# Performance work log

Measured on AMD Instinct MI355X. Metric: run time of the kernel, lower is better.

Reference implementation:

```python
import jax, jax.numpy as jnp
import numpy as np

DIM = 512
NUM_HEADS = 16
HEAD_DIM = DIM // NUM_HEADS
HIDDEN = int(DIM * 4.0)
EPS = 1e-5


def layer_norm(x, gamma, beta):
    mu = jnp.mean(x, axis=-1, keepdims=True)
    var = jnp.mean(jnp.square(x - mu), axis=-1, keepdims=True)
    return (x - mu) * jax.lax.rsqrt(var + EPS) * gamma + beta


def setup_inputs() -> dict:
    key = jax.random.key(0)
    ks = jax.random.split(key, 8)
    B, L, C = 32, 3136, DIM
    x = jax.random.normal(ks[0], (B, L, C), dtype=jnp.float32)
    norm1_g = jnp.ones((C,), jnp.float32)
    norm1_b = jnp.zeros((C,), jnp.float32)
    # spatial (per-head) mixing weight: (num_heads, head_dim, head_dim)
    w_spatial = jax.random.normal(ks[1], (NUM_HEADS, HEAD_DIM, HEAD_DIM), jnp.float32) * (1.0 / np.sqrt(HEAD_DIM))
    norm2_g = jnp.ones((C,), jnp.float32)
    norm2_b = jnp.zeros((C,), jnp.float32)
    w1 = jax.random.normal(ks[2], (C, HIDDEN), jnp.float32) * (1.0 / np.sqrt(C))
    b1 = jnp.zeros((HIDDEN,), jnp.float32)
    w2 = jax.random.normal(ks[3], (HIDDEN, C), jnp.float32) * (1.0 / np.sqrt(HIDDEN))
    b2 = jnp.zeros((C,), jnp.float32)
    return {"x": x, "norm1_g": norm1_g, "norm1_b": norm1_b, "w_spatial": w_spatial,
            "norm2_g": norm2_g, "norm2_b": norm2_b, "w1": w1, "b1": b1, "w2": w2, "b2": b2}


def reference(x, norm1_g, norm1_b, w_spatial, norm2_g, norm2_b, w1, b1, w2, b2):
    B, L, C = x.shape
    shortcut = x
    h = layer_norm(x, norm1_g, norm1_b)
    # window partition -> per-head channel-sub-dim linear (shared across windows/positions)
    # mathematically equivalent to applying the per-head matmul at every token
    h = h.reshape(B, L, NUM_HEADS, HEAD_DIM)
    h = jnp.einsum('blhd,hde->blhe', h, w_spatial)
    h = h.reshape(B, L, C)
    x = shortcut + h
    # channel MLP: Linear -> GELU(tanh) -> Linear
    y = layer_norm(x, norm2_g, norm2_b)
    y = jax.nn.gelu(y @ w1 + b1, approximate=True)
    y = y @ w2 + b2
    return x + y
```

## Files before the change

kernel.cpp:

```cpp
#include <hip/hip_runtime.h>
#include <hip/hip_bf16.h>


typedef __bf16 bf16x8 __attribute__((ext_vector_type(8)));
typedef float f32x4 __attribute__((ext_vector_type(4)));

constexpr int CDIM = 512;
constexpr int HID = 2048;
constexpr int MROWS = 32 * 3136;
constexpr float LN_EPS = 1e-5f;

static __device__ __forceinline__ float gelu_tanh(float x) {
  const float u = 0.7978845608028654f * fmaf(0.044715f * x * x, x, x);
  const float e = __expf(2.0f * u);
  return 0.5f * x * (2.0f - 2.0f / (e + 1.0f));
}

static __device__ __forceinline__ void load_lds16(const void* g, void* l) {
  __builtin_amdgcn_global_load_lds((__attribute__((address_space(1))) void*)g,
                                   (__attribute__((address_space(3))) void*)l,
                                   16, 0, 0);
}

template <int KD, int ND>
__global__ __launch_bounds__(256) void cvt_t(const float* __restrict__ src,
                                             __hip_bfloat16* __restrict__ dst) {
  __shared__ float tl[64][65];
  const int t = threadIdx.x;
  constexpr int NTN = ND / 64;
  const int k0 = (blockIdx.x / NTN) * 64;
  const int n0 = (blockIdx.x % NTN) * 64;
  const int c4 = (t & 15) * 4;
  const int r = t >> 4;
#pragma unroll
  for (int j = 0; j < 4; ++j) {
    const int kk = r + j * 16;
    const float4 v = *(const float4*)&src[(size_t)(k0 + kk) * ND + n0 + c4];
    tl[c4 + 0][kk] = v.x;
    tl[c4 + 1][kk] = v.y;
    tl[c4 + 2][kk] = v.z;
    tl[c4 + 3][kk] = v.w;
  }
  __syncthreads();
#pragma unroll
  for (int j = 0; j < 4; ++j) {
    const int nn = r + j * 16;
    __hip_bfloat16 o[4];
#pragma unroll
    for (int c = 0; c < 4; ++c) o[c] = __float2bfloat16(tl[nn][c4 + c]);
    *(uint2*)&dst[(size_t)(n0 + nn) * KD + k0 + c4] = *(const uint2*)o;
  }
}

__global__ __launch_bounds__(256) void fused_pre(
    const float* __restrict__ x, const float* __restrict__ g1,
    const float* __restrict__ b1, const float* __restrict__ wsp,
    const float* __restrict__ g2, const float* __restrict__ b2,
    float* __restrict__ x2out, __hip_bfloat16* __restrict__ yout) {
  __shared__ float lnbuf[2][CDIM];
  __shared__ float red[16];

  const int t = threadIdx.x;
  const int lane = t & 63;
  const int w = t >> 6;
  const int c0 = 2 * t;
  const int hd = c0 >> 5, e0 = c0 & 31;

  float wc0[32], wc1[32];
#pragma unroll
  for (int d = 0; d < 32; ++d) {
    const float2 wv = *(const float2*)&wsp[(hd * 32 + d) * 32 + e0];
    wc0[d] = wv.x;
    wc1[d] = wv.y;
  }
  const float2 g1v = *(const float2*)&g1[c0];
  const float2 b1v = *(const float2*)&b1[c0];
  const float2 g2v = *(const float2*)&g2[c0];
  const float2 b2v = *(const float2*)&b2[c0];

  for (int rp = blockIdx.x; rp < MROWS / 2; rp += gridDim.x) {
    const size_t ra = (size_t)rp * 2, rb = ra + 1;
    const float2 xa = *(const float2*)&x[ra * CDIM + c0];
    const float2 xb = *(const float2*)&x[rb * CDIM + c0];

    float sa = xa.x + xa.y, qa = xa.x * xa.x + xa.y * xa.y;
    float sb = xb.x + xb.y, qb = xb.x * xb.x + xb.y * xb.y;
#pragma unroll
    for (int off = 32; off; off >>= 1) {
      sa += __shfl_down(sa, off);
      qa += __shfl_down(qa, off);
      sb += __shfl_down(sb, off);
      qb += __shfl_down(qb, off);
    }
    if (lane == 0) {
      red[w * 4 + 0] = sa;
      red[w * 4 + 1] = qa;
      red[w * 4 + 2] = sb;
      red[w * 4 + 3] = qb;
    }
    __syncthreads();
    sa = red[0] + red[4] + red[8] + red[12];
    qa = red[1] + red[5] + red[9] + red[13];
    sb = red[2] + red[6] + red[10] + red[14];
    qb = red[3] + red[7] + red[11] + red[15];
    float mua = sa * (1.0f / CDIM), mub = sb * (1.0f / CDIM);
    float rsa = rsqrtf(qa * (1.0f / CDIM) - mua * mua + LN_EPS);
    float rsb = rsqrtf(qb * (1.0f / CDIM) - mub * mub + LN_EPS);
    lnbuf[0][c0] = (xa.x - mua) * rsa * g1v.x + b1v.x;
    lnbuf[0][c0 + 1] = (xa.y - mua) * rsa * g1v.y + b1v.y;
    lnbuf[1][c0] = (xb.x - mub) * rsb * g1v.x + b1v.x;
    lnbuf[1][c0 + 1] = (xb.y - mub) * rsb * g1v.y + b1v.y;
    __syncthreads();

    float ha0 = 0.f, ha1 = 0.f, hb0 = 0.f, hb1 = 0.f;
#pragma unroll
    for (int d = 0; d < 32; ++d) {
      const float la = lnbuf[0][hd * 32 + d];
      const float lb = lnbuf[1][hd * 32 + d];
      ha0 = fmaf(la, wc0[d], ha0);
      ha1 = fmaf(la, wc1[d], ha1);
      hb0 = fmaf(lb, wc0[d], hb0);
      hb1 = fmaf(lb, wc1[d], hb1);
    }
    const float a0 = xa.x + ha0, a1 = xa.y + ha1;
    const float b0 = xb.x + hb0, b1r = xb.y + hb1;
    float2 av;
    av.x = a0;
    av.y = a1;
    *(float2*)&x2out[ra * CDIM + c0] = av;
    av.x = b0;
    av.y = b1r;
    *(float2*)&x2out[rb * CDIM + c0] = av;

    sa = a0 + a1;
    qa = a0 * a0 + a1 * a1;
    sb = b0 + b1r;
    qb = b0 * b0 + b1r * b1r;
#pragma unroll
    for (int off = 32; off; off >>= 1) {
      sa += __shfl_down(sa, off);
      qa += __shfl_down(qa, off);
      sb += __shfl_down(sb, off);
      qb += __shfl_down(qb, off);
    }
    if (lane == 0) {
      red[w * 4 + 0] = sa;
      red[w * 4 + 1] = qa;
      red[w * 4 + 2] = sb;
      red[w * 4 + 3] = qb;
    }
    __syncthreads();
    sa = red[0] + red[4] + red[8] + red[12];
    qa = red[1] + red[5] + red[9] + red[13];
    sb = red[2] + red[6] + red[10] + red[14];
    qb = red[3] + red[7] + red[11] + red[15];
    mua = sa * (1.0f / CDIM);
    mub = sb * (1.0f / CDIM);
    rsa = rsqrtf(qa * (1.0f / CDIM) - mua * mua + LN_EPS);
    rsb = rsqrtf(qb * (1.0f / CDIM) - mub * mub + LN_EPS);
    __hip_bfloat162 yv;
    yv.x = __float2bfloat16((a0 - mua) * rsa * g2v.x + b2v.x);
    yv.y = __float2bfloat16((a1 - mua) * rsa * g2v.y + b2v.y);
    *(__hip_bfloat162*)&yout[ra * CDIM + c0] = yv;
    yv.x = __float2bfloat16((b0 - mub) * rsb * g2v.x + b2v.x);
    yv.y = __float2bfloat16((b1r - mub) * rsb * g2v.y + b2v.y);
    *(__hip_bfloat162*)&yout[rb * CDIM + c0] = yv;
    __syncthreads();
  }
}

template <int K, int N, bool GELU>
__global__ __launch_bounds__(256, 3) void gemmd2(
    const __hip_bfloat16* __restrict__ A, const __hip_bfloat16* __restrict__ Bt,
    const float* __restrict__ bias, __hip_bfloat16* __restrict__ zout,
    float* __restrict__ fout) {
  constexpr int NT = N / 128;
  constexpr int NKT = K / 32;
  __shared__ __attribute__((aligned(16))) char smem_raw[32768];

  const int tid = threadIdx.x;
  const int lane = tid & 63;
  const int w = tid >> 6;
  const int wr = w >> 1, wc = w & 1;

  const int cpx = gridDim.x >> 3;
  const int bid = (blockIdx.x & 7) * cpx + (blockIdx.x >> 3);
  const int tm = bid / NT, tn = bid - tm * NT;
  const size_t am0 = (size_t)tm * 128;
  const int bn0 = tn * 128;

  const int r0 = tid >> 2, q0 = tid & 3;
  const __hip_bfloat16* aP0 = A + (am0 + r0) * K + q0 * 8;
  const __hip_bfloat16* aP1 = aP0 + (size_t)64 * K;
  const __hip_bfloat16* bP0 = Bt + (size_t)(bn0 + r0) * K + q0 * 8;
  const __hip_bfloat16* bP1 = bP0 + (size_t)64 * K;
  const int wb = w * 1024;

  const int fr = lane & 15;
  const int kb = (lane >> 4) * 16;
  const int abase = (wr * 64 + fr) * 64 + kb;
  const int bbase = 8192 + (wc * 64 + fr) * 64 + kb;

#define STAGE(so, kt)                                          \
  do {                                                         \
    load_lds16(aP0 + (kt) * 32, smem_raw + (so) + wb);         \
    load_lds16(aP1 + (kt) * 32, smem_raw + (so) + 4096 + wb);  \
    load_lds16(bP0 + (kt) * 32, smem_raw + (so) + 8192 + wb);  \
    load_lds16(bP1 + (kt) * 32, smem_raw + (so) + 12288 + wb); \
  } while (0)

  f32x4 acc[4][4] = {};

  STAGE(0, 0);
  __syncthreads();

  for (int t = 0; t < NKT; ++t) {
    const int d = (t & 1) * 16384, dn = 16384 - d;
    if (t + 1 < NKT) STAGE(dn, t + 1);

    bf16x8 af[4], bf[4];
#pragma unroll
    for (int m = 0; m < 4; ++m)
      af[m] = *(const bf16x8*)(smem_raw + d + abase + m * 1024);
#pragma unroll
    for (int n = 0; n < 4; ++n)
      bf[n] = *(const bf16x8*)(smem_raw + d + bbase + n * 1024);
#pragma unroll
    for (int m = 0; m < 4; ++m)
#pragma unroll
      for (int n = 0; n < 4; ++n)
        acc[m][n] = __builtin_amdgcn_mfma_f32_16x16x32_bf16(af[m], bf[n],
                                                            acc[m][n], 0, 0, 0);
    __syncthreads();
  }
#undef STAGE

  const int cr = (lane >> 4) * 4;
  const int cc = lane & 15;
  char* smb = smem_raw;

  if constexpr (GELU) {
    __hip_bfloat16* ot = (__hip_bfloat16*)smb;
#pragma unroll
    for (int n = 0; n < 4; ++n) {
      const int col = wc * 64 + n * 16 + cc;
      const float bv = bias[bn0 + col];
#pragma unroll
      for (int m = 0; m < 4; ++m) {
        const int row = wr * 64 + m * 16 + cr;
#pragma unroll
        for (int j = 0; j < 4; ++j)
          ot[(row + j) * 128 + col] =
              __float2bfloat16(gelu_tanh(acc[m][n][j] + bv));
      }
    }
    __syncthreads();
#pragma unroll
    for (int it = 0; it < 8; ++it) {
      const int seg = it * 256 + tid;
      const int row = seg >> 4, cs = seg & 15;
      const uint4 v = *(const uint4*)(smb + seg * 16);
      *(uint4*)&zout[(am0 + row) * N + bn0 + cs * 8] = v;
    }
  } else {
    float* ot = (float*)smb;
#pragma unroll
    for (int p = 0; p < 2; ++p) {
      if (p) __syncthreads();
      if (wr == p) {
#pragma unroll
        for (int n = 0; n < 4; ++n) {
          const int col = wc * 64 + n * 16 + cc;
          const float bv = bias[bn0 + col];
#pragma unroll
          for (int m = 0; m < 4; ++m) {
            const int rl = m * 16 + cr;
#pragma unroll
            for (int j = 0; j < 4; ++j)
              ot[(rl + j) * 128 + col] = acc[m][n][j] + bv;
          }
        }
      }
      __syncthreads();
#pragma unroll
      for (int it = 0; it < 8; ++it) {
        const int seg = it * 256 + tid;
        const int row = seg >> 5, cs = seg & 31;
        const float4 lv = *(const float4*)(smb + seg * 16);
        float* gp = &fout[(am0 + p * 64 + row) * N + bn0 + cs * 4];
        float4 o = *(const float4*)gp;
        o.x += lv.x;
        o.y += lv.y;
        o.z += lv.z;
        o.w += lv.w;
        *(float4*)gp = o;
      }
    }
  }
}

extern "C" void kernel_launch(void* const* d_in, const int* in_sizes, int n_in,
                              void* d_out, int out_size, void* d_ws,
                              size_t ws_size, hipStream_t stream) {
  const float* x = (const float*)d_in[0];
  const float* n1g = (const float*)d_in[1];
  const float* n1b = (const float*)d_in[2];
  const float* wsp = (const float*)d_in[3];
  const float* n2g = (const float*)d_in[4];
  const float* n2b = (const float*)d_in[5];
  const float* w1 = (const float*)d_in[6];
  const float* b1 = (const float*)d_in[7];
  const float* w2 = (const float*)d_in[8];
  const float* b2 = (const float*)d_in[9];
  float* out = (float*)d_out;

  __hip_bfloat16* ybuf = (__hip_bfloat16*)d_ws;
  __hip_bfloat16* zbuf = ybuf + (size_t)MROWS * CDIM;
  __hip_bfloat16* w1t = zbuf + (size_t)MROWS * HID;
  __hip_bfloat16* w2t = w1t + (size_t)CDIM * HID;

  cvt_t<CDIM, HID><<<(CDIM / 64) * (HID / 64), 256, 0, stream>>>(w1, w1t);
  cvt_t<HID, CDIM><<<(HID / 64) * (CDIM / 64), 256, 0, stream>>>(w2, w2t);
  fused_pre<<<2048, 256, 0, stream>>>(x, n1g, n1b, wsp, n2g, n2b, out, ybuf);
  gemmd2<CDIM, HID, true><<<(MROWS / 128) * (HID / 128), 256, 0, stream>>>(
      ybuf, w1t, b1, zbuf, nullptr);
  gemmd2<HID, CDIM, false><<<(MROWS / 128) * (CDIM / 128), 256, 0, stream>>>(
      zbuf, w2t, b2, nullptr, out);
}
```

Before: 872.9 us.

## Pre-pack weights into MFMA fragment order and load B directly to registers

The weight conversion kernel now writes W1/W2 in a packed layout that matches the per-lane MFMA fragment order. The GEMMs then load B fragments straight from global memory into registers with one-step prefetch, so only A is staged in LDS. This halves the LDS traffic and the LDS buffer used per k-step. In exchange, B comes from global or L2 each iteration, possibly with more latency exposed, and register pressure rises.

```diff
diff --git a/kernel.cpp b/kernel.cpp
--- a/kernel.cpp
+++ b/kernel.cpp
@@ -23,33 +23,20 @@
 }
 
 template <int KD, int ND>
-__global__ __launch_bounds__(256) void cvt_t(const float* __restrict__ src,
-                                             __hip_bfloat16* __restrict__ dst) {
-  __shared__ float tl[64][65];
-  const int t = threadIdx.x;
-  constexpr int NTN = ND / 64;
-  const int k0 = (blockIdx.x / NTN) * 64;
-  const int n0 = (blockIdx.x % NTN) * 64;
-  const int c4 = (t & 15) * 4;
-  const int r = t >> 4;
-#pragma unroll
-  for (int j = 0; j < 4; ++j) {
-    const int kk = r + j * 16;
-    const float4 v = *(const float4*)&src[(size_t)(k0 + kk) * ND + n0 + c4];
-    tl[c4 + 0][kk] = v.x;
-    tl[c4 + 1][kk] = v.y;
-    tl[c4 + 2][kk] = v.z;
-    tl[c4 + 3][kk] = v.w;
-  }
-  __syncthreads();
-#pragma unroll
-  for (int j = 0; j < 4; ++j) {
-    const int nn = r + j * 16;
-    __hip_bfloat16 o[4];
-#pragma unroll
-    for (int c = 0; c < 4; ++c) o[c] = __float2bfloat16(tl[nn][c4 + c]);
-    *(uint2*)&dst[(size_t)(n0 + nn) * KD + k0 + c4] = *(const uint2*)o;
-  }
+__global__ __launch_bounds__(256) void cvt_pack(const float* __restrict__ src,
+                                                __hip_bfloat16* __restrict__ dst) {
+  constexpr int NKT = KD / 32;
+  const int o = blockIdx.x * 256 + threadIdx.x;
+  const int l = o & 63;
+  const int gt = o >> 6;
+  const int t = gt & (NKT - 1), g = gt / NKT;
+  const int n = g * 16 + (l & 15);
+  const int k0 = t * 32 + (l >> 4) * 8;
+  __hip_bfloat16 v[8];
+#pragma unroll
+  for (int j = 0; j < 8; ++j)
+    v[j] = __float2bfloat16(src[(size_t)(k0 + j) * ND + n]);
+  *(uint4*)(dst + (size_t)o * 8) = *(const uint4*)v;
 }
 
 __global__ __launch_bounds__(256) void fused_pre(
@@ -170,13 +157,13 @@
 }
 
 template <int K, int N, bool GELU>
-__global__ __launch_bounds__(256, 3) void gemmd2(
-    const __hip_bfloat16* __restrict__ A, const __hip_bfloat16* __restrict__ Bt,
+__global__ __launch_bounds__(256, 3) void gemmbs(
+    const __hip_bfloat16* __restrict__ A, const char* __restrict__ Bp,
     const float* __restrict__ bias, __hip_bfloat16* __restrict__ zout,
     float* __restrict__ fout) {
   constexpr int NT = N / 128;
   constexpr int NKT = K / 32;
-  __shared__ __attribute__((aligned(16))) char smem_raw[32768];
+  __shared__ __attribute__((aligned(16))) char smem[32768];
 
   const int tid = threadIdx.x;
   const int lane = tid & 63;
@@ -192,52 +179,59 @@
   const int r0 = tid >> 2, q0 = tid & 3;
   const __hip_bfloat16* aP0 = A + (am0 + r0) * K + q0 * 8;
   const __hip_bfloat16* aP1 = aP0 + (size_t)64 * K;
-  const __hip_bfloat16* bP0 = Bt + (size_t)(bn0 + r0) * K + q0 * 8;
-  const __hip_bfloat16* bP1 = bP0 + (size_t)64 * K;
   const int wb = w * 1024;
 
   const int fr = lane & 15;
   const int kb = (lane >> 4) * 16;
   const int abase = (wr * 64 + fr) * 64 + kb;
-  const int bbase = 8192 + (wc * 64 + fr) * 64 + kb;
-
-#define STAGE(so, kt)                                          \
-  do {                                                         \
-    load_lds16(aP0 + (kt) * 32, smem_raw + (so) + wb);         \
-    load_lds16(aP1 + (kt) * 32, smem_raw + (so) + 4096 + wb);  \
-    load_lds16(bP0 + (kt) * 32, smem_raw + (so) + 8192 + wb);  \
-    load_lds16(bP1 + (kt) * 32, smem_raw + (so) + 12288 + wb); \
+
+  const char* bBase = Bp + ((size_t)(tn * 8 + wc * 4) * NKT) * 1024 + lane * 16;
+
+#define STAGE_A(so, kt)                                       \
+  do {                                                        \
+    load_lds16(aP0 + (kt) * 32, smem + (so) + wb);            \
+    load_lds16(aP1 + (kt) * 32, smem + (so) + 4096 + wb);     \
   } while (0)
 
   f32x4 acc[4][4] = {};
-
-  STAGE(0, 0);
+  bf16x8 bf[4], bfn[4];
+
+  STAGE_A(0, 0);
+#pragma unroll
+  for (int n = 0; n < 4; ++n)
+    bf[n] = *(const bf16x8*)(bBase + ((size_t)n * NKT) * 1024);
   __syncthreads();
 
   for (int t = 0; t < NKT; ++t) {
-    const int d = (t & 1) * 16384, dn = 16384 - d;
-    if (t + 1 < NKT) STAGE(dn, t + 1);
-
-    bf16x8 af[4], bf[4];
+    const int d = (t & 1) * 8192, dn = 8192 - d;
+    if (t + 1 < NKT) {
+      STAGE_A(dn, t + 1);
+#pragma unroll
+      for (int n = 0; n < 4; ++n)
+        bfn[n] = *(const bf16x8*)(bBase + ((size_t)n * NKT + t + 1) * 1024);
+    }
+
+    bf16x8 af[4];
 #pragma unroll
     for (int m = 0; m < 4; ++m)
-      af[m] = *(const bf16x8*)(smem_raw + d + abase + m * 1024);
-#pragma unroll
-    for (int n = 0; n < 4; ++n)
-      bf[n] = *(const bf16x8*)(smem_raw + d + bbase + n * 1024);
+      af[m] = *(const bf16x8*)(smem + d + abase + m * 1024);
 #pragma unroll
     for (int m = 0; m < 4; ++m)
 #pragma unroll
       for (int n = 0; n < 4; ++n)
         acc[m][n] = __builtin_amdgcn_mfma_f32_16x16x32_bf16(af[m], bf[n],
                                                             acc[m][n], 0, 0, 0);
+    if (t + 1 < NKT) {
+#pragma unroll
+      for (int n = 0; n < 4; ++n) bf[n] = bfn[n];
+    }
     __syncthreads();
   }
-#undef STAGE
+#undef STAGE_A
 
   const int cr = (lane >> 4) * 4;
   const int cc = lane & 15;
-  char* smb = smem_raw;
+  char* smb = smem;
 
   if constexpr (GELU) {
     __hip_bfloat16* ot = (__hip_bfloat16*)smb;
@@ -316,14 +310,14 @@
 
   __hip_bfloat16* ybuf = (__hip_bfloat16*)d_ws;
   __hip_bfloat16* zbuf = ybuf + (size_t)MROWS * CDIM;
-  __hip_bfloat16* w1t = zbuf + (size_t)MROWS * HID;
-  __hip_bfloat16* w2t = w1t + (size_t)CDIM * HID;
-
-  cvt_t<CDIM, HID><<<(CDIM / 64) * (HID / 64), 256, 0, stream>>>(w1, w1t);
-  cvt_t<HID, CDIM><<<(HID / 64) * (CDIM / 64), 256, 0, stream>>>(w2, w2t);
+  __hip_bfloat16* w1p = zbuf + (size_t)MROWS * HID;
+  __hip_bfloat16* w2p = w1p + (size_t)CDIM * HID;
+
+  cvt_pack<CDIM, HID><<<512, 256, 0, stream>>>(w1, w1p);
+  cvt_pack<HID, CDIM><<<512, 256, 0, stream>>>(w2, w2p);
   fused_pre<<<2048, 256, 0, stream>>>(x, n1g, n1b, wsp, n2g, n2b, out, ybuf);
-  gemmd2<CDIM, HID, true><<<(MROWS / 128) * (HID / 128), 256, 0, stream>>>(
-      ybuf, w1t, b1, zbuf, nullptr);
-  gemmd2<HID, CDIM, false><<<(MROWS / 128) * (CDIM / 128), 256, 0, stream>>>(
-      zbuf, w2t, b2, nullptr, out);
-}
+  gemmbs<CDIM, HID, true><<<(MROWS / 128) * (HID / 128), 256, 0, stream>>>(
+      ybuf, (const char*)w1p, b1, zbuf, nullptr);
+  gemmbs<HID, CDIM, false><<<(MROWS / 128) * (CDIM / 128), 256, 0, stream>>>(
+      zbuf, (const char*)w2p, b2, nullptr, out);
+}
```

After: 880.6 us. About the same (+0.9%).
